# Performance work log

Measured on AMD Instinct MI355X. Metric: run time of the kernel, lower is better.

## Reference

```python
import jax, jax.numpy as jnp
import numpy as np

B, T, E, H, L = 2, 2048, 1024, 16, 4
HD = E // H
FF = 4 * E


def setup_inputs() -> dict:
    key = jax.random.key(0)
    ks = jax.random.split(key, 9)
    s = 0.02
    return {
        "x": jax.random.normal(ks[0], (B, T, E), dtype=jnp.float32),
        "Wqkv": jax.random.normal(ks[1], (L, E, 3 * E), dtype=jnp.float32) * s,
        "bqkv": jnp.zeros((L, 3 * E), dtype=jnp.float32),
        "Wproj": jax.random.normal(ks[2], (L, E, E), dtype=jnp.float32) * s,
        "bproj": jnp.zeros((L, E), dtype=jnp.float32),
        "W1": jax.random.normal(ks[3], (L, E, FF), dtype=jnp.float32) * s,
        "b1": jnp.zeros((L, FF), dtype=jnp.float32),
        "W2": jax.random.normal(ks[4], (L, FF, E), dtype=jnp.float32) * s,
        "b2": jnp.zeros((L, E), dtype=jnp.float32),
    }


def _attention(x, Wqkv_l, bqkv_l, Wproj_l, bproj_l):
    # (B,T,E) -> (B,T,E); manual softmax attention as in source
    qkv = x @ Wqkv_l + bqkv_l                      # (B,T,3E)
    q, k, v = jnp.split(qkv, 3, axis=-1)
    q = q.reshape(B, T, H, HD).transpose(0, 2, 1, 3)  # (B,H,T,HD)
    k = k.reshape(B, T, H, HD).transpose(0, 2, 1, 3)
    v = v.reshape(B, T, H, HD).transpose(0, 2, 1, 3)
    att = jnp.einsum("bhqd,bhkd->bhqk", q, k) * (1.0 / np.sqrt(HD))
    att = jax.nn.softmax(att, axis=-1)             # (B,H,T,T)
    y = jnp.einsum("bhqk,bhkd->bhqd", att, v)      # (B,H,T,HD)
    y = y.transpose(0, 2, 1, 3).reshape(B, T, E)
    return y @ Wproj_l + bproj_l


def reference(x, Wqkv, bqkv, Wproj, bproj, W1, b1, W2, b2):
    for l in range(L):
        x = x + _attention(x, Wqkv[l], bqkv[l], Wproj[l], bproj[l])  # residual x+f(x)
        h = jax.nn.gelu(x @ W1[l] + b1[l]) @ W2[l] + b2[l]           # MLP block
        x = x + h
    return x
```

## Files before the change

kernel.cpp:

```cpp
#include <hip/hip_runtime.h>
#include <hip/hip_bf16.h>

#define B_  2
#define T_  2048
#define E_  1024
#define H_  16
#define HD_ 64
#define FF_ 4096
#define L_  4
#define M_  (B_*T_)

typedef unsigned short u16;
typedef __attribute__((ext_vector_type(8))) short  short8;
typedef __attribute__((ext_vector_type(4))) float  f32x4;

#define QS 0.18033688011112042f

__device__ __forceinline__ u16 f2bf(float f) {
    union { float f; unsigned u; } v; v.f = f;
    unsigned r = (v.u + 0x7fffu + ((v.u >> 16) & 1u)) >> 16;
    return (u16)r;
}
__device__ __forceinline__ u16 f2bf_trunc(float f) {
    union { float f; unsigned u; } v; v.f = f;
    return (u16)(v.u >> 16);
}

__device__ __forceinline__ void gll16(const u16* g, u16* lds) {
    __builtin_amdgcn_global_load_lds(
        (const __attribute__((address_space(1))) unsigned int*)g,
        (__attribute__((address_space(3))) unsigned int*)lds, 16, 0, 0);
}

__global__ __launch_bounds__(256) void transpose_weights(
    const float* __restrict__ Wqkv, const float* __restrict__ Wproj,
    const float* __restrict__ W1,   const float* __restrict__ W2,
    u16* __restrict__ WT) {
    __shared__ float tile[32][33];
    int bid = blockIdx.x;
    const float* src; u16* dst; int K, N, lt;
    if (bid < 3072)      { src = Wqkv;  dst = WT;           K = 1024; N = 3072; lt = bid;        }
    else if (bid < 4096) { src = Wproj; dst = WT + 3145728; K = 1024; N = 1024; lt = bid - 3072; }
    else if (bid < 8192) { src = W1;    dst = WT + 4194304; K = 1024; N = 4096; lt = bid - 4096; }
    else                 { src = W2;    dst = WT + 8388608; K = 4096; N = 1024; lt = bid - 8192; }
    int tpr = N >> 5;
    int ti = lt / tpr, tj = lt % tpr;
    int k0 = ti << 5, n0 = tj << 5;
    int tx = threadIdx.x & 31, ty = threadIdx.x >> 5;
    for (int i = 0; i < 4; i++) {
        int r = ty + (i << 3);
        tile[r][tx] = src[(size_t)(k0 + r) * N + n0 + tx];
    }
    __syncthreads();
    for (int i = 0; i < 4; i++) {
        int r = ty + (i << 3);
        dst[(size_t)(n0 + r) * K + k0 + tx] = f2bf(tile[tx][r]);
    }
}

__global__ __launch_bounds__(256) void convert_kernel(
    const float* __restrict__ in, u16* __restrict__ out, int n4) {
    int i = blockIdx.x * 256 + threadIdx.x;
    if (i < n4) {
        float4 v = ((const float4*)in)[i];
        ushort4 w;
        w.x = f2bf(v.x); w.y = f2bf(v.y); w.z = f2bf(v.z); w.w = f2bf(v.w);
        ((ushort4*)out)[i] = w;
    }
}

template <int EPI>
__global__ __launch_bounds__(256) void gemm_kernel(
    const u16* __restrict__ A, const u16* __restrict__ Bt,
    const float* __restrict__ bias, void* outp, int M, int N, int K) {
    __shared__ u16 As[128 * 32];
    __shared__ u16 Bs[128 * 32];
    int t = threadIdx.x;
    int wid = t >> 6, lane = t & 63;
    int m0 = blockIdx.y << 7, n0 = blockIdx.x << 7;
    int l15 = t & 15, quad = (t >> 4) & 3;
    int wr = wid >> 1, wc = wid & 1;
    f32x4 acc[4][4];
#pragma unroll
    for (int i = 0; i < 4; i++)
#pragma unroll
        for (int j = 0; j < 4; j++) acc[i][j] = (f32x4){0.f, 0.f, 0.f, 0.f};

    int srow = (wid << 5) + (lane >> 2);
    int kch  = (((lane & 3) ^ ((lane >> 3) & 3)) << 3);
    const u16* gA = &A [(size_t)(m0 + srow) * K + kch];
    const u16* gB = &Bt[(size_t)(n0 + srow) * K + kch];
    int xo = (l15 >> 1) & 3;

    for (int k0 = 0; k0 < K; k0 += 32) {
        __syncthreads();
#pragma unroll
        for (int j = 0; j < 2; j++) {
            gll16(gA + (size_t)(j << 4) * K + k0, &As[((wid << 5) + (j << 4)) << 5]);
            gll16(gB + (size_t)(j << 4) * K + k0, &Bs[((wid << 5) + (j << 4)) << 5]);
        }
        __syncthreads();
        short8 af[4], bf[4];
#pragma unroll
        for (int i = 0; i < 4; i++)
            af[i] = *(const short8*)&As[((wr << 6) + (i << 4) + l15) * 32 + ((quad ^ xo) << 3)];
#pragma unroll
        for (int j = 0; j < 4; j++)
            bf[j] = *(const short8*)&Bs[((wc << 6) + (j << 4) + l15) * 32 + ((quad ^ xo) << 3)];
#pragma unroll
        for (int i = 0; i < 4; i++)
#pragma unroll
            for (int j = 0; j < 4; j++)
                acc[i][j] = __builtin_amdgcn_mfma_f32_16x16x32_bf16(af[i], bf[j], acc[i][j], 0, 0, 0);
    }
#pragma unroll
    for (int j = 0; j < 4; j++) {
        int gn = (n0 + (wc << 6) + (j << 4)) + l15;
        float bv = bias[gn];
#pragma unroll
        for (int i = 0; i < 4; i++) {
            int mb = m0 + (wr << 6) + (i << 4) + (quad << 2);
#pragma unroll
            for (int r = 0; r < 4; r++) {
                size_t idx = (size_t)(mb + r) * N + gn;
                float v = acc[i][j][r] + bv;
                if (EPI == 0) {
                    if (gn < E_) v *= QS;
                    ((u16*)outp)[idx] = f2bf(v);
                } else {
                    float u  = 0.7978845608028654f * (v + 0.044715f * v * v * v);
                    float th = 1.f - 2.f / (__expf(2.f * u) + 1.f);
                    ((u16*)outp)[idx] = f2bf(0.5f * v * (1.f + th));
                }
            }
        }
    }
}

__global__ __launch_bounds__(256) void gemm_n64(
    const u16* __restrict__ A, const u16* __restrict__ Bt,
    const float* __restrict__ bias, const float* __restrict__ res,
    float* __restrict__ outp, u16* __restrict__ out2, int M, int N, int K) {
    __shared__ u16 As[2][128 * 64];
    __shared__ u16 Bs[2][64 * 64];
    int t = threadIdx.x;
    int wid = t >> 6, lane = t & 63;
    int m0 = blockIdx.y << 7, n0 = blockIdx.x << 6;
    int l15 = t & 15, quad = (t >> 4) & 3;
    int wr = wid >> 1, wc = wid & 1;
    f32x4 acc[4][2];
#pragma unroll
    for (int i = 0; i < 4; i++)
#pragma unroll
        for (int j = 0; j < 2; j++) acc[i][j] = (f32x4){0.f, 0.f, 0.f, 0.f};

    int srow = lane >> 3;
    int kch  = (((lane & 7) ^ srow) << 3);
    const u16* gA = &A [(size_t)(m0 + (wid << 5) + srow) * K + kch];
    const u16* gB = &Bt[(size_t)(n0 + (wid << 4) + srow) * K + kch];
    int xo = l15 & 7;

    int nk = K >> 6;
#pragma unroll
    for (int g = 0; g < 4; g++)
        gll16(gA + (size_t)(g << 3) * K, &As[0][((wid << 5) + (g << 3)) << 6]);
#pragma unroll
    for (int g = 0; g < 2; g++)
        gll16(gB + (size_t)(g << 3) * K, &Bs[0][((wid << 4) + (g << 3)) << 6]);

    for (int kk = 0; kk < nk; kk++) {
        __syncthreads();
        int b = kk & 1;
        if (kk + 1 < nk) {
            int k1 = (kk + 1) << 6;
#pragma unroll
            for (int g = 0; g < 4; g++)
                gll16(gA + (size_t)(g << 3) * K + k1, &As[b ^ 1][((wid << 5) + (g << 3)) << 6]);
#pragma unroll
            for (int g = 0; g < 2; g++)
                gll16(gB + (size_t)(g << 3) * K + k1, &Bs[b ^ 1][((wid << 4) + (g << 3)) << 6]);
        }
        short8 af[2][4], bf[2][2];
#pragma unroll
        for (int kq = 0; kq < 2; kq++) {
            int ch = (((kq << 2) | quad) ^ xo) << 3;
#pragma unroll
            for (int i = 0; i < 4; i++)
                af[kq][i] = *(const short8*)&As[b][((wr << 6) + (i << 4) + l15) * 64 + ch];
#pragma unroll
            for (int j = 0; j < 2; j++)
                bf[kq][j] = *(const short8*)&Bs[b][((wc << 5) + (j << 4) + l15) * 64 + ch];
        }
#pragma unroll
        for (int kq = 0; kq < 2; kq++)
#pragma unroll
            for (int i = 0; i < 4; i++)
#pragma unroll
                for (int j = 0; j < 2; j++)
                    acc[i][j] = __builtin_amdgcn_mfma_f32_16x16x32_bf16(
                        af[kq][i], bf[kq][j], acc[i][j], 0, 0, 0);
    }
#pragma unroll
    for (int j = 0; j < 2; j++) {
        int gn = n0 + (wc << 5) + (j << 4) + l15;
        float bv = bias[gn];
#pragma unroll
        for (int i = 0; i < 4; i++) {
            int mb = m0 + (wr << 6) + (i << 4) + (quad << 2);
#pragma unroll
            for (int r = 0; r < 4; r++) {
                size_t idx = (size_t)(mb + r) * N + gn;
                float o = acc[i][j][r] + bv + res[idx];
                outp[idx] = o;
                out2[idx] = f2bf(o);
            }
        }
    }
}

__global__ __launch_bounds__(256) void attn_kernel(
    const u16* __restrict__ qkv, u16* __restrict__ y) {
    __shared__ u16 Qs[64 * 72];
    __shared__ u16 Ks[64 * 72];
    __shared__ u16 Vt[64 * 72];
    __shared__ u16 Pb[4 * 16 * 72];

    int t = threadIdx.x;
    int q0 = blockIdx.x << 6;
    int h  = blockIdx.y;
    int b  = blockIdx.z;
    const size_t rs = 3 * E_;
    const u16* base = qkv + (size_t)b * T_ * rs;

    {
        int r8 = t >> 3, dch = (t & 7) << 3;
#pragma unroll
        for (int p = 0; p < 2; p++) {
            int r = r8 + (p << 5);
            *(uint4*)&Qs[r * 72 + dch] =
                *(const uint4*)&base[(size_t)(q0 + r) * rs + h * 64 + dch];
        }
    }
    __syncthreads();
    int wid = t >> 6, l15 = t & 15, quad = (t >> 4) & 3;
    short8 qf0 = *(const short8*)&Qs[(wid * 16 + l15) * 72 + quad * 8];
    short8 qf1 = *(const short8*)&Qs[(wid * 16 + l15) * 72 + 32 + quad * 8];

    float m = -1e30f, l = 0.f;
    f32x4 o[4];
#pragma unroll
    for (int dt = 0; dt < 4; dt++) o[dt] = (f32x4){0.f, 0.f, 0.f, 0.f};

    int kkey = t >> 3, kch = (t & 7) << 3;
    int vkp = t & 31, vdc = t >> 5;

    for (int c0 = 0; c0 < T_; c0 += 64) {
#pragma unroll
        for (int p = 0; p < 2; p++) {
            int key = kkey + (p << 5);
            *(uint4*)&Ks[key * 72 + kch] =
                *(const uint4*)&base[(size_t)(c0 + key) * rs + E_ + h * 64 + kch];
        }
        {
            union { uint4 v; u16 u[8]; } v0, v1;
            v0.v = *(const uint4*)&base[(size_t)(c0 + 2 * vkp) * rs + 2 * E_ + h * 64 + (vdc << 3)];
            v1.v = *(const uint4*)&base[(size_t)(c0 + 2 * vkp + 1) * rs + 2 * E_ + h * 64 + (vdc << 3)];
#pragma unroll
            for (int i = 0; i < 8; i++) {
                unsigned pk = (unsigned)v0.u[i] | ((unsigned)v1.u[i] << 16);
                *(unsigned*)&Vt[(vdc * 8 + i) * 72 + 2 * vkp] = pk;
            }
        }
        __syncthreads();

        f32x4 s[4];
#pragma unroll
        for (int kt = 0; kt < 4; kt++) {
            short8 ka0 = *(const short8*)&Ks[(kt * 16 + l15) * 72 + quad * 8];
            short8 ka1 = *(const short8*)&Ks[(kt * 16 + l15) * 72 + 32 + quad * 8];
            f32x4 z = (f32x4){0.f, 0.f, 0.f, 0.f};
            z = __builtin_amdgcn_mfma_f32_16x16x32_bf16(ka0, qf0, z, 0, 0, 0);
            z = __builtin_amdgcn_mfma_f32_16x16x32_bf16(ka1, qf1, z, 0, 0, 0);
            s[kt] = z;
        }
        float cm = -1e30f;
#pragma unroll
        for (int kt = 0; kt < 4; kt++)
#pragma unroll
            for (int r = 0; r < 4; r++) cm = fmaxf(cm, s[kt][r]);
        cm = fmaxf(cm, __shfl_xor(cm, 16));
        cm = fmaxf(cm, __shfl_xor(cm, 32));
        float mn = fmaxf(m, cm);
        float alpha = exp2f(m - mn);
        float rsum = 0.f;
        float p[4][4];
#pragma unroll
        for (int kt = 0; kt < 4; kt++)
#pragma unroll
            for (int r = 0; r < 4; r++) {
                p[kt][r] = exp2f(s[kt][r] - mn);
                rsum += p[kt][r];
            }
        rsum += __shfl_xor(rsum, 16);
        rsum += __shfl_xor(rsum, 32);
        l = l * alpha + rsum;
        m = mn;
#pragma unroll
        for (int dt = 0; dt < 4; dt++)
#pragma unroll
            for (int r = 0; r < 4; r++) o[dt][r] *= alpha;

#pragma unroll
        for (int kt = 0; kt < 4; kt++) {
            ushort4 w;
            w.x = f2bf_trunc(p[kt][0]); w.y = f2bf_trunc(p[kt][1]);
            w.z = f2bf_trunc(p[kt][2]); w.w = f2bf_trunc(p[kt][3]);
            *(ushort4*)&Pb[(wid * 16 + l15) * 72 + kt * 16 + quad * 4] = w;
        }
        __threadfence_block();

        short8 pb0 = *(const short8*)&Pb[(wid * 16 + l15) * 72 + quad * 8];
        short8 pb1 = *(const short8*)&Pb[(wid * 16 + l15) * 72 + 32 + quad * 8];
#pragma unroll
        for (int dt = 0; dt < 4; dt++) {
            short8 vf0 = *(const short8*)&Vt[(dt * 16 + l15) * 72 + quad * 8];
            short8 vf1 = *(const short8*)&Vt[(dt * 16 + l15) * 72 + 32 + quad * 8];
            o[dt] = __builtin_amdgcn_mfma_f32_16x16x32_bf16(vf0, pb0, o[dt], 0, 0, 0);
            o[dt] = __builtin_amdgcn_mfma_f32_16x16x32_bf16(vf1, pb1, o[dt], 0, 0, 0);
        }
        __syncthreads();
    }
    float rl = 1.f / l;
    size_t yrow = ((size_t)b * T_ + q0 + wid * 16 + l15) * E_ + h * 64;
#pragma unroll
    for (int dt = 0; dt < 4; dt++) {
        ushort4 w;
        w.x = f2bf(o[dt][0] * rl); w.y = f2bf(o[dt][1] * rl);
        w.z = f2bf(o[dt][2] * rl); w.w = f2bf(o[dt][3] * rl);
        *(ushort4*)&y[yrow + dt * 16 + quad * 4] = w;
    }
}

extern "C" void kernel_launch(void* const* d_in, const int* in_sizes, int n_in,
                              void* d_out, int out_size, void* d_ws, size_t ws_size,
                              hipStream_t stream) {
    const float* x_in  = (const float*)d_in[0];
    const float* Wqkv  = (const float*)d_in[1];
    const float* bqkv  = (const float*)d_in[2];
    const float* Wproj = (const float*)d_in[3];
    const float* bproj = (const float*)d_in[4];
    const float* W1    = (const float*)d_in[5];
    const float* b1    = (const float*)d_in[6];
    const float* W2    = (const float*)d_in[7];
    const float* b2    = (const float*)d_in[8];
    float* out = (float*)d_out;

    u16* WT   = (u16*)d_ws;
    u16* qkvb = WT   + 12582912;
    u16* yb   = qkvb + 12582912;
    u16* hb   = yb   + 4194304;
    u16* xb   = hb   + 16777216;

    convert_kernel<<<4096, 256, 0, stream>>>(x_in, xb, M_ * E_ / 4);

    for (int l = 0; l < L_; l++) {
        transpose_weights<<<12288, 256, 0, stream>>>(
            Wqkv + (size_t)l * E_ * 3 * E_, Wproj + (size_t)l * E_ * E_,
            W1 + (size_t)l * E_ * FF_, W2 + (size_t)l * FF_ * E_, WT);

        const float* xcur = (l == 0) ? x_in : out;

        gemm_kernel<0><<<dim3(24, 32), 256, 0, stream>>>(
            xb, WT, bqkv + l * 3 * E_, qkvb, M_, 3 * E_, E_);

        attn_kernel<<<dim3(T_ / 64, H_, B_), 256, 0, stream>>>(qkvb, yb);

        gemm_n64<<<dim3(16, 32), 256, 0, stream>>>(
            yb, WT + 3145728, bproj + l * E_, xcur, out, xb, M_, E_, E_);

        gemm_kernel<2><<<dim3(32, 32), 256, 0, stream>>>(
            xb, WT + 4194304, b1 + l * FF_, hb, M_, FF_, E_);

        gemm_n64<<<dim3(16, 32), 256, 0, stream>>>(
            hb, WT + 8388608, b2 + l * E_, out, out, xb, M_, E_, FF_);
    }
}
```

Measured before the change: 1.345 ms.

## Double-buffer GEMM and attention LDS tiles with prefetch and XOR-swizzled layouts

The GEMM kernel now uses two LDS buffers and issues the global-to-LDS loads for the next K tile before computing on the current one, which removes one barrier per iteration. The attention kernel double-buffers its K and V^T tiles and prefetches the next key chunk while computing the current one. It also swaps padded LDS rows for XOR-swizzled 64-wide rows, loads Q straight from global into registers, and uses the hardware exp2 and rcp intrinsics. This aims to hide global load latency and cut LDS bank conflicts, at the cost of doubling LDS use and carrying more live registers for the prefetched V data.

```diff
diff --git a/kernel.cpp b/kernel.cpp
--- a/kernel.cpp
+++ b/kernel.cpp
@@ -9,6 +9,7 @@
 #define FF_ 4096
 #define L_  4
 #define M_  (B_*T_)
+#define RS_ (3*E_)
 
 typedef unsigned short u16;
 typedef __attribute__((ext_vector_type(8))) short  short8;
@@ -73,8 +74,8 @@
 __global__ __launch_bounds__(256) void gemm_kernel(
     const u16* __restrict__ A, const u16* __restrict__ Bt,
     const float* __restrict__ bias, void* outp, int M, int N, int K) {
-    __shared__ u16 As[128 * 32];
-    __shared__ u16 Bs[128 * 32];
+    __shared__ u16 As[2][128 * 32];
+    __shared__ u16 Bs[2][128 * 32];
     int t = threadIdx.x;
     int wid = t >> 6, lane = t & 63;
     int m0 = blockIdx.y << 7, n0 = blockIdx.x << 7;
@@ -91,22 +92,35 @@
     const u16* gA = &A [(size_t)(m0 + srow) * K + kch];
     const u16* gB = &Bt[(size_t)(n0 + srow) * K + kch];
     int xo = (l15 >> 1) & 3;
-
-    for (int k0 = 0; k0 < K; k0 += 32) {
+    int abase = (((wr << 6) + l15) << 5) + ((quad ^ xo) << 3);
+    int bbase = (((wc << 6) + l15) << 5) + ((quad ^ xo) << 3);
+
+    int nk = K >> 5;
+#pragma unroll
+    for (int g = 0; g < 2; g++) {
+        gll16(gA + (size_t)(g << 4) * K, &As[0][((wid << 5) + (g << 4)) << 5]);
+        gll16(gB + (size_t)(g << 4) * K, &Bs[0][((wid << 5) + (g << 4)) << 5]);
+    }
+    for (int kk = 0; kk < nk; kk++) {
         __syncthreads();
-#pragma unroll
-        for (int j = 0; j < 2; j++) {
-            gll16(gA + (size_t)(j << 4) * K + k0, &As[((wid << 5) + (j << 4)) << 5]);
-            gll16(gB + (size_t)(j << 4) * K + k0, &Bs[((wid << 5) + (j << 4)) << 5]);
-        }
-        __syncthreads();
+        const u16* as = &As[kk & 1][0];
+        const u16* bs = &Bs[kk & 1][0];
+        if (kk + 1 < nk) {
+            int k1 = (kk + 1) << 5;
+            int bn = (kk + 1) & 1;
+#pragma unroll
+            for (int g = 0; g < 2; g++) {
+                gll16(gA + (size_t)(g << 4) * K + k1, &As[bn][((wid << 5) + (g << 4)) << 5]);
+                gll16(gB + (size_t)(g << 4) * K + k1, &Bs[bn][((wid << 5) + (g << 4)) << 5]);
+            }
+        }
         short8 af[4], bf[4];
 #pragma unroll
         for (int i = 0; i < 4; i++)
-            af[i] = *(const short8*)&As[((wr << 6) + (i << 4) + l15) * 32 + ((quad ^ xo) << 3)];
+            af[i] = *(const short8*)(as + abase + (i << 9));
 #pragma unroll
         for (int j = 0; j < 4; j++)
-            bf[j] = *(const short8*)&Bs[((wc << 6) + (j << 4) + l15) * 32 + ((quad ^ xo) << 3)];
+            bf[j] = *(const short8*)(bs + bbase + (j << 9));
 #pragma unroll
         for (int i = 0; i < 4; i++)
 #pragma unroll
@@ -220,124 +234,141 @@
 
 __global__ __launch_bounds__(256) void attn_kernel(
     const u16* __restrict__ qkv, u16* __restrict__ y) {
-    __shared__ u16 Qs[64 * 72];
-    __shared__ u16 Ks[64 * 72];
-    __shared__ u16 Vt[64 * 72];
-    __shared__ u16 Pb[4 * 16 * 72];
+    __shared__ u16 Ks[2][64 * 64];
+    __shared__ u16 Vt[2][64 * 64];
+    __shared__ u16 Pb[4][16 * 64];
 
     int t = threadIdx.x;
     int q0 = blockIdx.x << 6;
     int h  = blockIdx.y;
     int b  = blockIdx.z;
-    const size_t rs = 3 * E_;
-    const u16* base = qkv + (size_t)b * T_ * rs;
-
-    {
-        int r8 = t >> 3, dch = (t & 7) << 3;
-#pragma unroll
-        for (int p = 0; p < 2; p++) {
-            int r = r8 + (p << 5);
-            *(uint4*)&Qs[r * 72 + dch] =
-                *(const uint4*)&base[(size_t)(q0 + r) * rs + h * 64 + dch];
-        }
-    }
-    __syncthreads();
-    int wid = t >> 6, l15 = t & 15, quad = (t >> 4) & 3;
-    short8 qf0 = *(const short8*)&Qs[(wid * 16 + l15) * 72 + quad * 8];
-    short8 qf1 = *(const short8*)&Qs[(wid * 16 + l15) * 72 + 32 + quad * 8];
+    const u16* bq = qkv + (size_t)b * T_ * RS_;
+
+    int wid = t >> 6, lane = t & 63, l15 = t & 15, quad = (t >> 4) & 3;
+    int sw = l15 & 7;
+    int ro0 = (l15 << 6) + ((quad ^ sw) << 3);
+    int ro1 = ro0 ^ 32;
+    int krow = (wid << 4) + (lane >> 3);
+    size_t kg0 = (size_t)krow * RS_ + E_ + h * 64 + (((lane & 7) ^ (lane >> 3)) << 3);
+    int vkp = t & 31, vdc = t >> 5;
+    size_t vg0 = (size_t)(2 * vkp) * RS_ + 2 * E_ + h * 64 + (vdc << 3);
+    int vwo[8];
+#pragma unroll
+    for (int i = 0; i < 8; i++)
+        vwo[i] = (((vdc << 3) + i) << 6) + ((((vkp >> 2) ^ i)) << 3) + ((vkp & 3) << 1);
+    int pwo[4];
+#pragma unroll
+    for (int kt = 0; kt < 4; kt++)
+        pwo[kt] = (l15 << 6) + ((((kt << 1) | (quad >> 1)) ^ sw) << 3) + ((quad & 1) << 2);
+    u16* pw = &Pb[wid][0];
+
+    const u16* qp = bq + (size_t)(q0 + (wid << 4) + l15) * RS_ + h * 64;
+    short8 qf0 = *(const short8*)(qp + (quad << 3));
+    short8 qf1 = *(const short8*)(qp + (quad << 3) + 32);
 
     float m = -1e30f, l = 0.f;
     f32x4 o[4];
 #pragma unroll
     for (int dt = 0; dt < 4; dt++) o[dt] = (f32x4){0.f, 0.f, 0.f, 0.f};
 
-    int kkey = t >> 3, kch = (t & 7) << 3;
-    int vkp = t & 31, vdc = t >> 5;
-
-    for (int c0 = 0; c0 < T_; c0 += 64) {
-#pragma unroll
-        for (int p = 0; p < 2; p++) {
-            int key = kkey + (p << 5);
-            *(uint4*)&Ks[key * 72 + kch] =
-                *(const uint4*)&base[(size_t)(c0 + key) * rs + E_ + h * 64 + kch];
-        }
-        {
-            union { uint4 v; u16 u[8]; } v0, v1;
-            v0.v = *(const uint4*)&base[(size_t)(c0 + 2 * vkp) * rs + 2 * E_ + h * 64 + (vdc << 3)];
-            v1.v = *(const uint4*)&base[(size_t)(c0 + 2 * vkp + 1) * rs + 2 * E_ + h * 64 + (vdc << 3)];
-#pragma unroll
-            for (int i = 0; i < 8; i++) {
-                unsigned pk = (unsigned)v0.u[i] | ((unsigned)v1.u[i] << 16);
-                *(unsigned*)&Vt[(vdc * 8 + i) * 72 + 2 * vkp] = pk;
-            }
-        }
-        __syncthreads();
-
-        f32x4 s[4];
-#pragma unroll
-        for (int kt = 0; kt < 4; kt++) {
-            short8 ka0 = *(const short8*)&Ks[(kt * 16 + l15) * 72 + quad * 8];
-            short8 ka1 = *(const short8*)&Ks[(kt * 16 + l15) * 72 + 32 + quad * 8];
-            f32x4 z = (f32x4){0.f, 0.f, 0.f, 0.f};
-            z = __builtin_amdgcn_mfma_f32_16x16x32_bf16(ka0, qf0, z, 0, 0, 0);
-            z = __builtin_amdgcn_mfma_f32_16x16x32_bf16(ka1, qf1, z, 0, 0, 0);
-            s[kt] = z;
-        }
-        float cm = -1e30f;
-#pragma unroll
-        for (int kt = 0; kt < 4; kt++)
-#pragma unroll
-            for (int r = 0; r < 4; r++) cm = fmaxf(cm, s[kt][r]);
-        cm = fmaxf(cm, __shfl_xor(cm, 16));
-        cm = fmaxf(cm, __shfl_xor(cm, 32));
-        float mn = fmaxf(m, cm);
-        float alpha = exp2f(m - mn);
-        float rsum = 0.f;
-        float p[4][4];
-#pragma unroll
-        for (int kt = 0; kt < 4; kt++)
-#pragma unroll
-            for (int r = 0; r < 4; r++) {
-                p[kt][r] = exp2f(s[kt][r] - mn);
-                rsum += p[kt][r];
-            }
-        rsum += __shfl_xor(rsum, 16);
-        rsum += __shfl_xor(rsum, 32);
-        l = l * alpha + rsum;
-        m = mn;
-#pragma unroll
-        for (int dt = 0; dt < 4; dt++)
-#pragma unroll
-            for (int r = 0; r < 4; r++) o[dt][r] *= alpha;
-
-#pragma unroll
-        for (int kt = 0; kt < 4; kt++) {
-            ushort4 w;
-            w.x = f2bf_trunc(p[kt][0]); w.y = f2bf_trunc(p[kt][1]);
-            w.z = f2bf_trunc(p[kt][2]); w.w = f2bf_trunc(p[kt][3]);
-            *(ushort4*)&Pb[(wid * 16 + l15) * 72 + kt * 16 + quad * 4] = w;
-        }
-        __threadfence_block();
-
-        short8 pb0 = *(const short8*)&Pb[(wid * 16 + l15) * 72 + quad * 8];
-        short8 pb1 = *(const short8*)&Pb[(wid * 16 + l15) * 72 + 32 + quad * 8];
-#pragma unroll
-        for (int dt = 0; dt < 4; dt++) {
-            short8 vf0 = *(const short8*)&Vt[(dt * 16 + l15) * 72 + quad * 8];
-            short8 vf1 = *(const short8*)&Vt[(dt * 16 + l15) * 72 + 32 + quad * 8];
-            o[dt] = __builtin_amdgcn_mfma_f32_16x16x32_bf16(vf0, pb0, o[dt], 0, 0, 0);
-            o[dt] = __builtin_amdgcn_mfma_f32_16x16x32_bf16(vf1, pb1, o[dt], 0, 0, 0);
-        }
-        __syncthreads();
-    }
-    float rl = 1.f / l;
-    size_t yrow = ((size_t)b * T_ + q0 + wid * 16 + l15) * E_ + h * 64;
+    gll16(bq + kg0,            &Ks[0][(wid << 4) << 6]);
+    gll16(bq + kg0 + 8 * RS_,  &Ks[0][((wid << 4) + 8) << 6]);
+    {
+        union { uint4 q; u16 u[8]; } a_, b_;
+        a_.q = *(const uint4*)(bq + vg0);
+        b_.q = *(const uint4*)(bq + vg0 + RS_);
+#pragma unroll
+        for (int i = 0; i < 8; i++) {
+            unsigned pk = (unsigned)a_.u[i] | ((unsigned)b_.u[i] << 16);
+            *(unsigned*)(&Vt[0][0] + vwo[i]) = pk;
+        }
+    }
+
+#define ATTN_CHUNK(KSB, VTB, KSN, VTN, C0) do {                                \
+    __syncthreads();                           \
+    int cn_ = (C0) + 64;                                                       \
+    uint4 v0_, v1_;                                                            \
+    bool pf_ = (cn_ < T_);                                                     \
+    if (pf_) {                                                                 \
+        size_t cb_ = (size_t)cn_ * RS_;                                        \
+        gll16(bq + cb_ + kg0,           (KSN) + ((wid << 4) << 6));            \
+        gll16(bq + cb_ + kg0 + 8 * RS_, (KSN) + (((wid << 4) + 8) << 6));      \
+        v0_ = *(const uint4*)(bq + cb_ + vg0);                                 \
+        v1_ = *(const uint4*)(bq + cb_ + vg0 + RS_);                           \
+    }                                                                          \
+    f32x4 s_[4];                                                               \
+    _Pragma("unroll")                                                          \
+    for (int kt = 0; kt < 4; kt++) {                                           \
+        short8 ka0 = *(const short8*)((KSB) + (kt << 10) + ro0);               \
+        short8 ka1 = *(const short8*)((KSB) + (kt << 10) + ro1);               \
+        f32x4 z = (f32x4){0.f, 0.f, 0.f, 0.f};                                 \
+        z = __builtin_amdgcn_mfma_f32_16x16x32_bf16(ka0, qf0, z, 0, 0, 0);     \
+        z = __builtin_amdgcn_mfma_f32_16x16x32_bf16(ka1, qf1, z, 0, 0, 0);     \
+        s_[kt] = z;                                                            \
+    }                                                                          \
+    float cm_ = -1e30f;                                                        \
+    _Pragma("unroll")                                                          \
+    for (int kt = 0; kt < 4; kt++)                                             \
+        _Pragma("unroll")                                                      \
+        for (int r = 0; r < 4; r++) cm_ = fmaxf(cm_, s_[kt][r]);               \
+    cm_ = fmaxf(cm_, __shfl_xor(cm_, 16));                                     \
+    cm_ = fmaxf(cm_, __shfl_xor(cm_, 32));                                     \
+    float mn_ = fmaxf(m, cm_);                                                 \
+    float alpha_ = __builtin_amdgcn_exp2f(m - mn_);                            \
+    float rsum_ = 0.f;                                                         \
+    _Pragma("unroll")                                                          \
+    for (int kt = 0; kt < 4; kt++) {                                           \
+        float p0_ = __builtin_amdgcn_exp2f(s_[kt][0] - mn_);                   \
+        float p1_ = __builtin_amdgcn_exp2f(s_[kt][1] - mn_);                   \
+        float p2_ = __builtin_amdgcn_exp2f(s_[kt][2] - mn_);                   \
+        float p3_ = __builtin_amdgcn_exp2f(s_[kt][3] - mn_);                   \
+        rsum_ += (p0_ + p1_) + (p2_ + p3_);                                    \
+        ushort4 w_;                                                            \
+        w_.x = f2bf_trunc(p0_); w_.y = f2bf_trunc(p1_);                        \
+        w_.z = f2bf_trunc(p2_); w_.w = f2bf_trunc(p3_);                        \
+        *(ushort4*)(pw + pwo[kt]) = w_;                                        \
+    }                                                                          \
+    rsum_ += __shfl_xor(rsum_, 16);                                            \
+    rsum_ += __shfl_xor(rsum_, 32);                                            \
+    l = l * alpha_ + rsum_;                                                    \
+    m = mn_;                                                                   \
+    __threadfence_block();                   \
+    short8 pb0 = *(const short8*)(pw + ro0);                                   \
+    short8 pb1 = *(const short8*)(pw + ro1);                                   \
+    _Pragma("unroll")                                                          \
+    for (int dt = 0; dt < 4; dt++) {                                           \
+        _Pragma("unroll")                                                      \
+        for (int r = 0; r < 4; r++) o[dt][r] *= alpha_;                        \
+        short8 vf0 = *(const short8*)((VTB) + (dt << 10) + ro0);               \
+        short8 vf1 = *(const short8*)((VTB) + (dt << 10) + ro1);               \
+        o[dt] = __builtin_amdgcn_mfma_f32_16x16x32_bf16(vf0, pb0, o[dt], 0, 0, 0); \
+        o[dt] = __builtin_amdgcn_mfma_f32_16x16x32_bf16(vf1, pb1, o[dt], 0, 0, 0); \
+    }                                                                          \
+    if (pf_) {                                                                 \
+        union { uint4 q; u16 u[8]; } a_, b_;                                   \
+        a_.q = v0_; b_.q = v1_;                                                \
+        _Pragma("unroll")                                                      \
+        for (int i = 0; i < 8; i++) {                                          \
+            unsigned pk_ = (unsigned)a_.u[i] | ((unsigned)b_.u[i] << 16);      \
+            *(unsigned*)((VTN) + vwo[i]) = pk_;                                \
+        }                                                                      \
+    }                                                                          \
+} while (0)
+
+    for (int c0 = 0; c0 < T_; c0 += 128) {
+        ATTN_CHUNK(&Ks[0][0], &Vt[0][0], &Ks[1][0], &Vt[1][0], c0);
+        ATTN_CHUNK(&Ks[1][0], &Vt[1][0], &Ks[0][0], &Vt[0][0], c0 + 64);
+    }
+#undef ATTN_CHUNK
+
+    float rl = __builtin_amdgcn_rcpf(l);
+    size_t yrow = ((size_t)b * T_ + q0 + (wid << 4) + l15) * E_ + h * 64;
 #pragma unroll
     for (int dt = 0; dt < 4; dt++) {
         ushort4 w;
         w.x = f2bf(o[dt][0] * rl); w.y = f2bf(o[dt][1] * rl);
         w.z = f2bf(o[dt][2] * rl); w.w = f2bf(o[dt][3] * rl);
-        *(ushort4*)&y[yrow + dt * 16 + quad * 4] = w;
+        *(ushort4*)&y[yrow + (dt << 4) + (quad << 2)] = w;
     }
 }
 
```

Result: faster. 1.197 ms (-11.0%).
